# Kernel tuning notes

Measured on AMD Instinct MI355X. Metric: run time of the kernel, lower is better.

The kernel has to match this reference:

```python
import jax, jax.numpy as jnp
import numpy as np

EMB_DIM = 768
HEAD_SIZE = 64


def setup_inputs() -> dict:
    key = jax.random.key(0)
    kx, kk, kq, kv = jax.random.split(key, 4)
    B, S = 8, 2048
    bound = 1.0 / np.sqrt(EMB_DIM)  # torch Linear default init range
    x = jax.random.normal(kx, (B, S, EMB_DIM), dtype=jnp.float32)
    Wk = jax.random.uniform(kk, (EMB_DIM, HEAD_SIZE), jnp.float32, -bound, bound)
    Wq = jax.random.uniform(kq, (EMB_DIM, HEAD_SIZE), jnp.float32, -bound, bound)
    Wv = jax.random.uniform(kv, (EMB_DIM, HEAD_SIZE), jnp.float32, -bound, bound)
    return {"x": x, "Wk": Wk, "Wq": Wq, "Wv": Wv}


def reference(x, Wk, Wq, Wv):
    # bias-free projections: [b, s, d] @ [d, h] -> [b, s, h]
    key = jnp.einsum("bsd,dh->bsh", x, Wk)
    query = jnp.einsum("bsd,dh->bsh", x, Wq)
    value = jnp.einsum("bsd,dh->bsh", x, Wv)
    scale = 1.0 / jnp.sqrt(jnp.asarray(HEAD_SIZE, dtype=x.dtype))
    # [b, q, k] attention scores
    scores = jnp.einsum("bqh,bkh->bqk", query, key) * scale
    probs = jax.nn.softmax(scores, axis=-1)
    # weighted value sum: [b, q, h]
    out = jnp.einsum("bqk,bkh->bqh", probs, value)
    return out
```

## Files before the change

kernel.cpp:

```cpp
#include <hip/hip_runtime.h>
#include <hip/hip_bf16.h>
#include <stdint.h>

#define B_ 8
#define S_ 2048
#define D_ 768
#define H_ 64
#define M_ (B_*S_)

typedef __attribute__((ext_vector_type(8))) short bf16x8;
typedef __attribute__((ext_vector_type(4))) float f32x4;
typedef __attribute__((ext_vector_type(4))) float floatv4;
typedef __attribute__((ext_vector_type(4))) unsigned short u16x4;
typedef __attribute__((ext_vector_type(8))) unsigned short u16x8;

__device__ __forceinline__ uint16_t f2bf(float f) {
    union { float f; uint32_t u; } c; c.f = f;
    return (uint16_t)((c.u + 0x7FFFu + ((c.u >> 16) & 1u)) >> 16);
}

__device__ __forceinline__ void load_lds16(const void* g, void* l) {
    __builtin_amdgcn_global_load_lds(
        (const __attribute__((address_space(1))) uint32_t*)(const uint32_t*)g,
        (__attribute__((address_space(3))) uint32_t*)(uint32_t*)l,
        16, 0, 0);
}

__global__ __launch_bounds__(256) void k_convert_x(const float* __restrict__ x,
                                                   uint16_t* __restrict__ xb) {
    size_t i = ((size_t)blockIdx.x * 256 + threadIdx.x) * 8;
    floatv4 v0 = *(const floatv4*)(x + i);
    floatv4 v1 = *(const floatv4*)(x + i + 4);
    u16x8 o;
    o[0] = f2bf(v0[0]); o[1] = f2bf(v0[1]); o[2] = f2bf(v0[2]); o[3] = f2bf(v0[3]);
    o[4] = f2bf(v1[0]); o[5] = f2bf(v1[1]); o[6] = f2bf(v1[2]); o[7] = f2bf(v1[3]);
    *(u16x8*)(xb + i) = o;
}

__global__ __launch_bounds__(256) void k_convert_w(const float* __restrict__ Wk,
                                                   const float* __restrict__ Wq,
                                                   const float* __restrict__ Wv,
                                                   uint16_t* __restrict__ wt) {
    const int mat = blockIdx.y;
    const float* W = mat == 0 ? Wk : (mat == 1 ? Wq : Wv);
    const float scale = (mat == 1) ? 0.125f : 1.0f;
    uint16_t* out = wt + (size_t)mat * (H_ * D_);
    int i = blockIdx.x * 256 + threadIdx.x;
    int d = i >> 6, h = i & 63;
    out[h * D_ + d] = f2bf(W[i] * scale);
}

__global__ __launch_bounds__(256) void k_proj(const uint16_t* __restrict__ xb,
                                              const uint16_t* __restrict__ wt,
                                              uint16_t* __restrict__ kb,
                                              uint16_t* __restrict__ qb,
                                              uint16_t* __restrict__ vt) {
    __shared__ char lds[24576];
    const int tid  = threadIdx.x;
    const int lane = tid & 63, wave = tid >> 6;
    const int l15  = lane & 15, g = lane >> 4;
    const int m0   = blockIdx.x * 128;
    const int mat  = blockIdx.y;
    const uint16_t* wmat = wt + (size_t)mat * (H_ * D_);

    const int rloc = wave * 8 + (lane >> 3);
    const int cswz = (((lane & 7) ^ (lane >> 3)) << 4);
    const int wr = wave >> 1, wc = wave & 1;

    f32x4 acc[4][2] = {};

    for (int kt = 0; kt < 12; ++kt) {
#pragma unroll
        for (int j = 0; j < 4; ++j) {
            const char* src = (const char*)(xb + (size_t)(m0 + j*32 + rloc) * D_ + kt*64) + cswz;
            load_lds16(src, lds + j*4096 + wave*1024);
        }
#pragma unroll
        for (int j = 0; j < 2; ++j) {
            const char* src = (const char*)(wmat + (size_t)(j*32 + rloc) * D_ + kt*64) + cswz;
            load_lds16(src, lds + 16384 + j*4096 + wave*1024);
        }
        __syncthreads();

        bf16x8 a[4][2], b[2][2];
#pragma unroll
        for (int m = 0; m < 4; ++m)
#pragma unroll
            for (int kk = 0; kk < 2; ++kk) {
                int row = wr*64 + m*16 + l15;
                int cb  = (kk*64 + g*16) ^ ((row & 7) << 4);
                a[m][kk] = *(const bf16x8*)(lds + row*128 + cb);
            }
#pragma unroll
        for (int n = 0; n < 2; ++n)
#pragma unroll
            for (int kk = 0; kk < 2; ++kk) {
                int row = wc*32 + n*16 + l15;
                int cb  = (kk*64 + g*16) ^ ((row & 7) << 4);
                b[n][kk] = *(const bf16x8*)(lds + 16384 + row*128 + cb);
            }
#pragma unroll
        for (int m = 0; m < 4; ++m)
#pragma unroll
            for (int n = 0; n < 2; ++n)
#pragma unroll
                for (int kk = 0; kk < 2; ++kk)
                    acc[m][n] = __builtin_amdgcn_mfma_f32_16x16x32_bf16(
                                    a[m][kk], b[n][kk], acc[m][n], 0, 0, 0);
        __syncthreads();
    }

    if (mat < 2) {
        uint16_t* out = (mat == 0) ? kb : qb;
#pragma unroll
        for (int m = 0; m < 4; ++m)
#pragma unroll
            for (int n = 0; n < 2; ++n) {
                int col  = wc*32 + n*16 + l15;
                int row0 = m0 + wr*64 + m*16 + g*4;
#pragma unroll
                for (int r = 0; r < 4; ++r)
                    out[(size_t)(row0 + r) * H_ + col] = f2bf(acc[m][n][r]);
            }
    } else {
#pragma unroll
        for (int m = 0; m < 4; ++m)
#pragma unroll
            for (int n = 0; n < 2; ++n) {
                int col  = wc*32 + n*16 + l15;
                int row0 = m0 + wr*64 + m*16 + g*4;
                int bb = row0 >> 11, s = row0 & 2047;
                u16x4 pk;
#pragma unroll
                for (int r = 0; r < 4; ++r) pk[r] = f2bf(acc[m][n][r]);
                *(u16x4*)(vt + ((size_t)bb * H_ + col) * S_ + s) = pk;
            }
    }
}

__global__ __launch_bounds__(256) void k_attn(const uint16_t* __restrict__ qb,
                                              const uint16_t* __restrict__ kb,
                                              const uint16_t* __restrict__ vt,
                                              float* __restrict__ out) {
    __shared__ char plds[4][4096];
    __shared__ float o_buf[4 * 32 * 64];
    __shared__ float m_buf[4][32];
    __shared__ float l_buf[4][32];
    const int tid  = threadIdx.x;
    const int lane = tid & 63, wave = tid >> 6;
    const int l15 = lane & 15, g = lane >> 4;
    const int batch = blockIdx.y;
    const int q0 = blockIdx.x * 32;
    const size_t qrow = (size_t)batch * S_ + q0;

    bf16x8 aq[2][2];
#pragma unroll
    for (int qm = 0; qm < 2; ++qm)
#pragma unroll
        for (int kk = 0; kk < 2; ++kk)
            aq[qm][kk] = *(const bf16x8*)(qb + (qrow + qm*16 + l15) * H_ + kk*32 + g*8);

    f32x4 o[2][4] = {};
    float Mx[2][4], Ls[2][4];
#pragma unroll
    for (int qm = 0; qm < 2; ++qm)
#pragma unroll
        for (int r = 0; r < 4; ++r) { Mx[qm][r] = -3e38f; Ls[qm][r] = 0.f; }

    const uint16_t* kbase = kb + (size_t)batch * S_ * H_;
    const uint16_t* vbase = vt + (size_t)batch * H_ * S_;
    char* pl = plds[wave];

    for (int kt = wave * 8; kt < wave * 8 + 8; ++kt) {
        bf16x8 bk[4][2];
#pragma unroll
        for (int n = 0; n < 4; ++n)
#pragma unroll
            for (int kk = 0; kk < 2; ++kk)
                bk[n][kk] = *(const bf16x8*)(kbase + (size_t)(kt*64 + n*16 + l15) * H_ + kk*32 + g*8);
        f32x4 s[2][4] = {};
#pragma unroll
        for (int qm = 0; qm < 2; ++qm)
#pragma unroll
            for (int n = 0; n < 4; ++n)
#pragma unroll
                for (int kk = 0; kk < 2; ++kk)
                    s[qm][n] = __builtin_amdgcn_mfma_f32_16x16x32_bf16(
                                   aq[qm][kk], bk[n][kk], s[qm][n], 0, 0, 0);

#pragma unroll
        for (int qm = 0; qm < 2; ++qm) {
            float tm[4];
#pragma unroll
            for (int r = 0; r < 4; ++r)
                tm[r] = fmaxf(fmaxf(s[qm][0][r], s[qm][1][r]),
                              fmaxf(s[qm][2][r], s[qm][3][r]));
#pragma unroll
            for (int off = 1; off < 16; off <<= 1)
#pragma unroll
                for (int r = 0; r < 4; ++r)
                    tm[r] = fmaxf(tm[r], __shfl_xor(tm[r], off));
#pragma unroll
            for (int r = 0; r < 4; ++r) {
                float Mn = fmaxf(Mx[qm][r], tm[r]);
                float al = __expf(Mx[qm][r] - Mn);
                Mx[qm][r] = Mn;
                Ls[qm][r] *= al;
#pragma unroll
                for (int nh = 0; nh < 4; ++nh) o[qm][nh][r] *= al;
#pragma unroll
                for (int n = 0; n < 4; ++n) {
                    float p = __expf(s[qm][n][r] - Mn);
                    Ls[qm][r] += p;
                    int row = qm*16 + g*4 + r;
                    int cb  = ((n*16 + l15) * 2) ^ ((row & 7) << 4);
                    *(uint16_t*)(pl + row*128 + cb) = f2bf(p);
                }
            }
        }

        bf16x8 pa[2][2];
#pragma unroll
        for (int qm = 0; qm < 2; ++qm)
#pragma unroll
            for (int kk = 0; kk < 2; ++kk) {
                int row = qm*16 + l15;
                int cb  = (kk*64 + g*16) ^ ((row & 7) << 4);
                pa[qm][kk] = *(const bf16x8*)(pl + row*128 + cb);
            }
        bf16x8 bv[4][2];
#pragma unroll
        for (int nh = 0; nh < 4; ++nh)
#pragma unroll
            for (int kk = 0; kk < 2; ++kk)
                bv[nh][kk] = *(const bf16x8*)(vbase + (size_t)(nh*16 + l15) * S_ + kt*64 + kk*32 + g*8);
#pragma unroll
        for (int qm = 0; qm < 2; ++qm)
#pragma unroll
            for (int nh = 0; nh < 4; ++nh)
#pragma unroll
                for (int kk = 0; kk < 2; ++kk)
                    o[qm][nh] = __builtin_amdgcn_mfma_f32_16x16x32_bf16(
                                    pa[qm][kk], bv[nh][kk], o[qm][nh], 0, 0, 0);
    }

    if (l15 == 0) {
#pragma unroll
        for (int qm = 0; qm < 2; ++qm)
#pragma unroll
            for (int r = 0; r < 4; ++r)
                m_buf[wave][qm*16 + g*4 + r] = Mx[qm][r];
    }
    __syncthreads();

    float lrow[2][4];
#pragma unroll
    for (int qm = 0; qm < 2; ++qm)
#pragma unroll
        for (int r = 0; r < 4; ++r) {
            int row = qm*16 + g*4 + r;
            float ms = fmaxf(fmaxf(m_buf[0][row], m_buf[1][row]),
                             fmaxf(m_buf[2][row], m_buf[3][row]));
            float f = __expf(Mx[qm][r] - ms);
            float l = Ls[qm][r];
#pragma unroll
            for (int off = 1; off < 16; off <<= 1) l += __shfl_xor(l, off);
            lrow[qm][r] = l * f;
#pragma unroll
            for (int nh = 0; nh < 4; ++nh) o[qm][nh][r] *= f;
        }

    if (l15 == 0) {
#pragma unroll
        for (int qm = 0; qm < 2; ++qm)
#pragma unroll
            for (int r = 0; r < 4; ++r)
                l_buf[wave][qm*16 + g*4 + r] = lrow[qm][r];
    }
#pragma unroll
    for (int qm = 0; qm < 2; ++qm)
#pragma unroll
        for (int nh = 0; nh < 4; ++nh)
#pragma unroll
            for (int r = 0; r < 4; ++r) {
                int i = qm*16 + nh*4 + r;
                o_buf[(wave*32 + i)*64 + lane] = o[qm][nh][r];
            }
    __syncthreads();

    const int iw0 = wave * 8;
    const int qm0 = iw0 >> 4;
    float rinv[4];
#pragma unroll
    for (int r = 0; r < 4; ++r) {
        int row = qm0*16 + g*4 + r;
        rinv[r] = 1.0f / (l_buf[0][row] + l_buf[1][row] + l_buf[2][row] + l_buf[3][row]);
    }
    float* obase = out + qrow * H_;
#pragma unroll
    for (int ii = 0; ii < 8; ++ii) {
        int i = iw0 + ii;
        int nh = (i >> 2) & 3, r = i & 3;
        float tot = o_buf[(0*32 + i)*64 + lane] + o_buf[(1*32 + i)*64 + lane]
                  + o_buf[(2*32 + i)*64 + lane] + o_buf[(3*32 + i)*64 + lane];
        int row = qm0*16 + g*4 + r, col = nh*16 + l15;
        obase[(size_t)row * H_ + col] = tot * rinv[r];
    }
}

extern "C" void kernel_launch(void* const* d_in, const int* in_sizes, int n_in,
                              void* d_out, int out_size, void* d_ws, size_t ws_size,
                              hipStream_t stream) {
    const float* x  = (const float*)d_in[0];
    const float* Wk = (const float*)d_in[1];
    const float* Wq = (const float*)d_in[2];
    const float* Wv = (const float*)d_in[3];
    float* out = (float*)d_out;

    uint16_t* ws = (uint16_t*)d_ws;
    uint16_t* xb = ws;
    uint16_t* wt = xb + (size_t)M_ * D_;
    uint16_t* kb = wt + (size_t)3 * H_ * D_;
    uint16_t* qb = kb + (size_t)M_ * H_;
    uint16_t* vt = qb + (size_t)M_ * H_;

    k_convert_x<<<dim3(M_ * D_ / 2048), dim3(256), 0, stream>>>(x, xb);
    k_convert_w<<<dim3(192, 3), dim3(256), 0, stream>>>(Wk, Wq, Wv, wt);
    k_proj<<<dim3(M_ / 128, 3), dim3(256), 0, stream>>>(xb, wt, kb, qb, vt);
    k_attn<<<dim3(S_ / 32, B_), dim3(256), 0, stream>>>(qb, kb, vt, out);
}
```

Before: 138.4 us.

## Fuse x conversion into projection, compute QKV per block, lazy softmax rescale

Removes the separate fp32-to-bf16 pass over x by loading fp32 x directly in the projection kernel and converting into LDS, with double-buffered register/LDS prefetch. One block now computes all three K/Q/V projections for its rows, so x is read once instead of three times. In attention, log2(e) is folded into the Q scale so the kernel can use exp2f, the rescale of the running max is skipped unless the max grows by more than 8, and V loads are issued earlier to overlap with the softmax. The projection now uses 64 KB of LDS and 512-thread blocks, which may reduce occupancy. The lazy rescale relies on bf16/fp32 headroom to stay accurate.

```diff
diff --git a/kernel.cpp b/kernel.cpp
--- a/kernel.cpp
+++ b/kernel.cpp
@@ -24,17 +24,6 @@
         (const __attribute__((address_space(1))) uint32_t*)(const uint32_t*)g,
         (__attribute__((address_space(3))) uint32_t*)(uint32_t*)l,
         16, 0, 0);
-}
-
-__global__ __launch_bounds__(256) void k_convert_x(const float* __restrict__ x,
-                                                   uint16_t* __restrict__ xb) {
-    size_t i = ((size_t)blockIdx.x * 256 + threadIdx.x) * 8;
-    floatv4 v0 = *(const floatv4*)(x + i);
-    floatv4 v1 = *(const floatv4*)(x + i + 4);
-    u16x8 o;
-    o[0] = f2bf(v0[0]); o[1] = f2bf(v0[1]); o[2] = f2bf(v0[2]); o[3] = f2bf(v0[3]);
-    o[4] = f2bf(v1[0]); o[5] = f2bf(v1[1]); o[6] = f2bf(v1[2]); o[7] = f2bf(v1[3]);
-    *(u16x8*)(xb + i) = o;
 }
 
 __global__ __launch_bounds__(256) void k_convert_w(const float* __restrict__ Wk,
@@ -43,99 +32,118 @@
                                                    uint16_t* __restrict__ wt) {
     const int mat = blockIdx.y;
     const float* W = mat == 0 ? Wk : (mat == 1 ? Wq : Wv);
-    const float scale = (mat == 1) ? 0.125f : 1.0f;
+    const float scale = (mat == 1) ? 0.18033688011f : 1.0f;
     uint16_t* out = wt + (size_t)mat * (H_ * D_);
     int i = blockIdx.x * 256 + threadIdx.x;
     int d = i >> 6, h = i & 63;
     out[h * D_ + d] = f2bf(W[i] * scale);
 }
 
-__global__ __launch_bounds__(256) void k_proj(const uint16_t* __restrict__ xb,
+__global__ __launch_bounds__(512) void k_proj(const float* __restrict__ x,
                                               const uint16_t* __restrict__ wt,
                                               uint16_t* __restrict__ kb,
                                               uint16_t* __restrict__ qb,
                                               uint16_t* __restrict__ vt) {
-    __shared__ char lds[24576];
+    __shared__ char lds[65536];
     const int tid  = threadIdx.x;
     const int lane = tid & 63, wave = tid >> 6;
     const int l15  = lane & 15, g = lane >> 4;
-    const int m0   = blockIdx.x * 128;
-    const int mat  = blockIdx.y;
-    const uint16_t* wmat = wt + (size_t)mat * (H_ * D_);
-
-    const int rloc = wave * 8 + (lane >> 3);
+    const int m0   = blockIdx.x * 64;
+    const int mrow = (wave >> 1) * 16;
+    const int nb   = (wave & 1) * 32;
+
+    const int trow = tid >> 3, tc8 = tid & 7;
+    const float* xrowp = x + (size_t)(m0 + trow) * D_ + tc8 * 8;
+    const int xw = trow * 128 + ((tc8 ^ (trow & 7)) << 4);
+
     const int cswz = (((lane & 7) ^ (lane >> 3)) << 4);
-    const int wr = wave >> 1, wc = wave & 1;
-
-    f32x4 acc[4][2] = {};
+    const char* wsrc[3];
+    int wdst[3];
+#pragma unroll
+    for (int j = 0; j < 3; ++j) {
+        int c = wave * 3 + j, mat = c >> 3, wrow = (c & 7) * 8 + (lane >> 3);
+        wsrc[j] = (const char*)(wt + (size_t)mat * (H_ * D_) + (size_t)wrow * D_) + cswz;
+        wdst[j] = 16384 + c * 1024;
+    }
+
+    floatv4 xr0 = *(const floatv4*)(xrowp);
+    floatv4 xr1 = *(const floatv4*)(xrowp + 4);
+#pragma unroll
+    for (int j = 0; j < 3; ++j)
+        load_lds16(wsrc[j], lds + wdst[j]);
+    {
+        u16x8 cv;
+        cv[0]=f2bf(xr0[0]); cv[1]=f2bf(xr0[1]); cv[2]=f2bf(xr0[2]); cv[3]=f2bf(xr0[3]);
+        cv[4]=f2bf(xr1[0]); cv[5]=f2bf(xr1[1]); cv[6]=f2bf(xr1[2]); cv[7]=f2bf(xr1[3]);
+        *(u16x8*)(lds + xw) = cv;
+    }
+    __syncthreads();
+
+    f32x4 acc[3][2] = {};
 
     for (int kt = 0; kt < 12; ++kt) {
-#pragma unroll
-        for (int j = 0; j < 4; ++j) {
-            const char* src = (const char*)(xb + (size_t)(m0 + j*32 + rloc) * D_ + kt*64) + cswz;
-            load_lds16(src, lds + j*4096 + wave*1024);
-        }
-#pragma unroll
-        for (int j = 0; j < 2; ++j) {
-            const char* src = (const char*)(wmat + (size_t)(j*32 + rloc) * D_ + kt*64) + cswz;
-            load_lds16(src, lds + 16384 + j*4096 + wave*1024);
+        const int cur = kt & 1, nxt = cur ^ 1;
+        if (kt < 11) {
+            xr0 = *(const floatv4*)(xrowp + (kt + 1) * 64);
+            xr1 = *(const floatv4*)(xrowp + (kt + 1) * 64 + 4);
+#pragma unroll
+            for (int j = 0; j < 3; ++j)
+                load_lds16(wsrc[j] + (size_t)(kt + 1) * 128, lds + nxt * 24576 + wdst[j]);
+        }
+        const char* xsb = lds + cur * 8192;
+        const char* wsb = lds + 16384 + cur * 24576;
+        bf16x8 a[2], b[3][2][2];
+#pragma unroll
+        for (int kk = 0; kk < 2; ++kk) {
+            int row = mrow + l15;
+            a[kk] = *(const bf16x8*)(xsb + row * 128 + ((kk*64 + g*16) ^ ((row & 7) << 4)));
+        }
+#pragma unroll
+        for (int mat = 0; mat < 3; ++mat)
+#pragma unroll
+            for (int n = 0; n < 2; ++n)
+#pragma unroll
+                for (int kk = 0; kk < 2; ++kk) {
+                    int row = nb + n * 16 + l15;
+                    b[mat][n][kk] = *(const bf16x8*)(wsb + mat * 8192 + row * 128 +
+                                                     ((kk*64 + g*16) ^ ((row & 7) << 4)));
+                }
+#pragma unroll
+        for (int mat = 0; mat < 3; ++mat)
+#pragma unroll
+            for (int n = 0; n < 2; ++n)
+#pragma unroll
+                for (int kk = 0; kk < 2; ++kk)
+                    acc[mat][n] = __builtin_amdgcn_mfma_f32_16x16x32_bf16(
+                                      a[kk], b[mat][n][kk], acc[mat][n], 0, 0, 0);
+        if (kt < 11) {
+            u16x8 cv;
+            cv[0]=f2bf(xr0[0]); cv[1]=f2bf(xr0[1]); cv[2]=f2bf(xr0[2]); cv[3]=f2bf(xr0[3]);
+            cv[4]=f2bf(xr1[0]); cv[5]=f2bf(xr1[1]); cv[6]=f2bf(xr1[2]); cv[7]=f2bf(xr1[3]);
+            *(u16x8*)(lds + nxt * 8192 + xw) = cv;
         }
         __syncthreads();
-
-        bf16x8 a[4][2], b[2][2];
-#pragma unroll
-        for (int m = 0; m < 4; ++m)
-#pragma unroll
-            for (int kk = 0; kk < 2; ++kk) {
-                int row = wr*64 + m*16 + l15;
-                int cb  = (kk*64 + g*16) ^ ((row & 7) << 4);
-                a[m][kk] = *(const bf16x8*)(lds + row*128 + cb);
-            }
-#pragma unroll
-        for (int n = 0; n < 2; ++n)
-#pragma unroll
-            for (int kk = 0; kk < 2; ++kk) {
-                int row = wc*32 + n*16 + l15;
-                int cb  = (kk*64 + g*16) ^ ((row & 7) << 4);
-                b[n][kk] = *(const bf16x8*)(lds + 16384 + row*128 + cb);
-            }
-#pragma unroll
-        for (int m = 0; m < 4; ++m)
-#pragma unroll
-            for (int n = 0; n < 2; ++n)
-#pragma unroll
-                for (int kk = 0; kk < 2; ++kk)
-                    acc[m][n] = __builtin_amdgcn_mfma_f32_16x16x32_bf16(
-                                    a[m][kk], b[n][kk], acc[m][n], 0, 0, 0);
-        __syncthreads();
-    }
-
-    if (mat < 2) {
-        uint16_t* out = (mat == 0) ? kb : qb;
-#pragma unroll
-        for (int m = 0; m < 4; ++m)
-#pragma unroll
-            for (int n = 0; n < 2; ++n) {
-                int col  = wc*32 + n*16 + l15;
-                int row0 = m0 + wr*64 + m*16 + g*4;
+    }
+
+#pragma unroll
+    for (int mat = 0; mat < 3; ++mat)
+#pragma unroll
+        for (int n = 0; n < 2; ++n) {
+            int col  = nb + n * 16 + l15;
+            int row0 = m0 + mrow + g * 4;
+            if (mat < 2) {
+                uint16_t* out = (mat == 0) ? kb : qb;
 #pragma unroll
                 for (int r = 0; r < 4; ++r)
-                    out[(size_t)(row0 + r) * H_ + col] = f2bf(acc[m][n][r]);
-            }
-    } else {
-#pragma unroll
-        for (int m = 0; m < 4; ++m)
-#pragma unroll
-            for (int n = 0; n < 2; ++n) {
-                int col  = wc*32 + n*16 + l15;
-                int row0 = m0 + wr*64 + m*16 + g*4;
+                    out[(size_t)(row0 + r) * H_ + col] = f2bf(acc[mat][n][r]);
+            } else {
                 int bb = row0 >> 11, s = row0 & 2047;
                 u16x4 pk;
 #pragma unroll
-                for (int r = 0; r < 4; ++r) pk[r] = f2bf(acc[m][n][r]);
+                for (int r = 0; r < 4; ++r) pk[r] = f2bf(acc[mat][n][r]);
                 *(u16x4*)(vt + ((size_t)bb * H_ + col) * S_ + s) = pk;
             }
-    }
+        }
 }
 
 __global__ __launch_bounds__(256) void k_attn(const uint16_t* __restrict__ qb,
@@ -188,6 +196,13 @@
                     s[qm][n] = __builtin_amdgcn_mfma_f32_16x16x32_bf16(
                                    aq[qm][kk], bk[n][kk], s[qm][n], 0, 0, 0);
 
+        bf16x8 bv[4][2];
+#pragma unroll
+        for (int nh = 0; nh < 4; ++nh)
+#pragma unroll
+            for (int kk = 0; kk < 2; ++kk)
+                bv[nh][kk] = *(const bf16x8*)(vbase + (size_t)(nh*16 + l15) * S_ + kt*64 + kk*32 + g*8);
+
 #pragma unroll
         for (int qm = 0; qm < 2; ++qm) {
             float tm[4];
@@ -202,15 +217,17 @@
                     tm[r] = fmaxf(tm[r], __shfl_xor(tm[r], off));
 #pragma unroll
             for (int r = 0; r < 4; ++r) {
-                float Mn = fmaxf(Mx[qm][r], tm[r]);
-                float al = __expf(Mx[qm][r] - Mn);
-                Mx[qm][r] = Mn;
-                Ls[qm][r] *= al;
-#pragma unroll
-                for (int nh = 0; nh < 4; ++nh) o[qm][nh][r] *= al;
+                if (tm[r] > Mx[qm][r] + 8.0f) {
+                    float al = exp2f(Mx[qm][r] - tm[r]);
+                    Mx[qm][r] = tm[r];
+                    Ls[qm][r] *= al;
+#pragma unroll
+                    for (int nh = 0; nh < 4; ++nh) o[qm][nh][r] *= al;
+                }
+                float Mn = Mx[qm][r];
 #pragma unroll
                 for (int n = 0; n < 4; ++n) {
-                    float p = __expf(s[qm][n][r] - Mn);
+                    float p = exp2f(s[qm][n][r] - Mn);
                     Ls[qm][r] += p;
                     int row = qm*16 + g*4 + r;
                     int cb  = ((n*16 + l15) * 2) ^ ((row & 7) << 4);
@@ -228,12 +245,6 @@
                 int cb  = (kk*64 + g*16) ^ ((row & 7) << 4);
                 pa[qm][kk] = *(const bf16x8*)(pl + row*128 + cb);
             }
-        bf16x8 bv[4][2];
-#pragma unroll
-        for (int nh = 0; nh < 4; ++nh)
-#pragma unroll
-            for (int kk = 0; kk < 2; ++kk)
-                bv[nh][kk] = *(const bf16x8*)(vbase + (size_t)(nh*16 + l15) * S_ + kt*64 + kk*32 + g*8);
 #pragma unroll
         for (int qm = 0; qm < 2; ++qm)
 #pragma unroll
@@ -261,7 +272,7 @@
             int row = qm*16 + g*4 + r;
             float ms = fmaxf(fmaxf(m_buf[0][row], m_buf[1][row]),
                              fmaxf(m_buf[2][row], m_buf[3][row]));
-            float f = __expf(Mx[qm][r] - ms);
+            float f = exp2f(Mx[qm][r] - ms);
             float l = Ls[qm][r];
 #pragma unroll
             for (int off = 1; off < 16; off <<= 1) l += __shfl_xor(l, off);
@@ -318,14 +329,12 @@
     float* out = (float*)d_out;
 
     uint16_t* ws = (uint16_t*)d_ws;
-    uint16_t* xb = ws;
-    uint16_t* wt = xb + (size_t)M_ * D_;
+    uint16_t* wt = ws;
     uint16_t* kb = wt + (size_t)3 * H_ * D_;
     uint16_t* qb = kb + (size_t)M_ * H_;
     uint16_t* vt = qb + (size_t)M_ * H_;
 
-    k_convert_x<<<dim3(M_ * D_ / 2048), dim3(256), 0, stream>>>(x, xb);
     k_convert_w<<<dim3(192, 3), dim3(256), 0, stream>>>(Wk, Wq, Wv, wt);
-    k_proj<<<dim3(M_ / 128, 3), dim3(256), 0, stream>>>(xb, wt, kb, qb, vt);
+    k_proj<<<dim3(M_ / 64), dim3(512), 0, stream>>>(x, wt, kb, qb, vt);
     k_attn<<<dim3(S_ / 32, B_), dim3(256), 0, stream>>>(qb, kb, vt, out);
 }
```

Result: faster. 131.4 us (-5.1%).
